# Performance work log

Hardware: AMD Instinct MI355X
Metric: run time of the kernel (lower is better)

## Reference

```python
import jax, jax.numpy as jnp
import numpy as np

B, F, T = 64, 256, 1024  # batch, input features, time steps
H, O = 1024, 512         # hidden units, output projection dim


def setup_inputs() -> dict:
    key = jax.random.key(0)
    k = jax.random.split(key, 4)
    scale_x = 1.0 / np.sqrt(F)
    scale_h = 1.0 / np.sqrt(H)
    return {
        "x": jax.random.normal(k[0], (B, F, T), dtype=jnp.float32),
        "Wx": jax.random.normal(k[1], (F, H), dtype=jnp.float32) * scale_x,
        "Wh": jax.random.normal(k[2], (H, H), dtype=jnp.float32) * scale_h,
        "b": jnp.zeros((H,), dtype=jnp.float32),
        "Wout": jax.random.normal(k[3], (H, O), dtype=jnp.float32) * scale_h,
        "bout": jnp.zeros((O,), dtype=jnp.float32),
    }


def reference(x, Wx, Wh, b, Wout, bout):
    # inputs are (B, F, T); tf.unstack(axis=-1) -> per-step (B, F) slices
    xT = jnp.moveaxis(x, -1, 0)  # (T, B, F)
    s0 = jnp.zeros((x.shape[0], Wh.shape[0]), dtype=x.dtype)

    def step(state, xt):
        # simple RNN cell: tanh(x@Wx + s@Wh + b)
        new_state = jnp.tanh(xt @ Wx + state @ Wh + b)
        return new_state, new_state

    _, states = jax.lax.scan(step, s0, xT)       # (T, B, H)
    states = jnp.moveaxis(states, 0, 1)          # (B, T, H) -- tf.stack(axis=1)
    out = states @ Wout + bout                   # per-timestep Dense projection
    return out
```

## Files before the change

### kernel.cpp

```cpp
#include <hip/hip_runtime.h>
#include <math.h>

#define B_ 64
#define F_ 256
#define T_ 1024
#define H_ 1024
#define O_ 512

#define NCHAIN 4
#define NMEM   16

#define S3_T 65536

typedef short short8 __attribute__((ext_vector_type(8)));
typedef float f32x4 __attribute__((ext_vector_type(4)));
typedef unsigned int uint4v __attribute__((ext_vector_type(4)));
typedef unsigned long long ull;

__device__ inline float bf2f(unsigned short u) {
    union { unsigned int i; float f; } v; v.i = ((unsigned int)u) << 16; return v.f;
}
__device__ inline unsigned short f2bf(float f) {
    union { float f; unsigned int i; } v; v.f = f;
    unsigned int i = v.i;
    unsigned int r = (i + 0x7fffu + ((i >> 16) & 1u)) >> 16;
    return (unsigned short)r;
}

__global__ void wt_transpose(const float* __restrict__ src,
                             unsigned short* __restrict__ dst, int K, int N) {
    __shared__ float tile[32][33];
    int n0 = blockIdx.x * 32, k0 = blockIdx.y * 32;
    int tx = threadIdx.x, ty = threadIdx.y;
    for (int i = ty; i < 32; i += 8)
        tile[i][tx] = src[(size_t)(k0 + i) * N + n0 + tx];
    __syncthreads();
    for (int i = ty; i < 32; i += 8)
        dst[(size_t)(n0 + i) * K + k0 + tx] = f2bf(tile[tx][i]);
}

__global__ void xpose_x(const float* __restrict__ x, unsigned short* __restrict__ xT) {
    __shared__ float tile[64][65];
    int id = blockIdx.x;
    int b = id >> 6;
    int ft = (id >> 4) & 3;
    int tt = id & 15;
    int f0 = ft * 64, t0 = tt * 64;
    for (int i = threadIdx.x; i < 64 * 64; i += 256) {
        int fl = i >> 6, tl = i & 63;
        tile[fl][tl] = x[((size_t)(b * F_ + f0 + fl)) * T_ + t0 + tl];
    }
    __syncthreads();
    for (int i = threadIdx.x; i < 64 * 64; i += 256) {
        int tl = i >> 6, fl = i & 63;
        xT[((size_t)(t0 + tl) * B_ + b) * F_ + f0 + fl] = f2bf(tile[fl][tl]);
    }
}

__global__ __launch_bounds__(256) void proj_kernel(
    const unsigned short* __restrict__ xT, const unsigned short* __restrict__ WxT,
    const float* __restrict__ bias, unsigned short* __restrict__ S) {
    int nb = blockIdx.x;
    int mb = blockIdx.y;
    int wave = threadIdx.x >> 6, lane = threadIdx.x & 63;
    int col16 = lane & 15, quad = lane >> 4;
    int m0 = mb * 64 + wave * 16;
    int n0 = nb * 64;

    f32x4 acc[4];
    for (int s = 0; s < 4; ++s)
        for (int r = 0; r < 4; ++r) acc[s][r] = 0.0f;

    #pragma unroll
    for (int kc = 0; kc < F_ / 32; ++kc) {
        int k0 = kc * 32 + quad * 8;
        short8 a = *reinterpret_cast<const short8*>(xT + (size_t)(m0 + col16) * F_ + k0);
        #pragma unroll
        for (int s = 0; s < 4; ++s) {
            short8 bfr = *reinterpret_cast<const short8*>(
                WxT + (size_t)(n0 + s * 16 + col16) * F_ + k0);
            acc[s] = __builtin_amdgcn_mfma_f32_16x16x32_bf16(a, bfr, acc[s], 0, 0, 0);
        }
    }
    #pragma unroll
    for (int s = 0; s < 4; ++s) {
        int col = n0 + s * 16 + col16;
        float bb = bias[col];
        #pragma unroll
        for (int r = 0; r < 4; ++r) {
            int brow = wave * 16 + quad * 4 + r;
            size_t off = (size_t)mb * S3_T + (size_t)(brow >> 4) * 16384 +
                         (size_t)(col >> 6) * 1024 + (brow & 15) * 64 + (col & 63);
            S[off] = f2bf(acc[s][r] + bb);
        }
    }
}

__global__ void init_ctrl(unsigned int* ctrl) {
    for (int i = threadIdx.x; i < 8192; i += 256) ctrl[i] = 0u;
}

template<bool LOCAL>
__device__ __forceinline__ void st_h(unsigned short* p, unsigned short v) {
    if (LOCAL) {
        *p = v;
    } else {
        asm volatile("global_store_short %0, %1, off sc0 sc1"
                     :: "v"((ull)(uintptr_t)p), "v"((unsigned int)v) : "memory");
    }
}

template<bool LOCAL>
__device__ __forceinline__ void flag_store(unsigned int* p, unsigned int v) {
    if (LOCAL) {
        asm volatile("global_atomic_swap %0, %1, off"
                     :: "v"((ull)(uintptr_t)p), "v"(v) : "memory");
    } else {
        __hip_atomic_store(p, v, __ATOMIC_RELAXED, __HIP_MEMORY_SCOPE_AGENT);
    }
}

template<bool LOCAL>
__device__ __forceinline__ unsigned int flag_load(unsigned int* p) {
    unsigned int old;
    if (LOCAL) {
        asm volatile("global_atomic_add %0, %1, %2, off sc0\n\t"
                     "s_waitcnt vmcnt(0)"
                     : "=v"(old) : "v"((ull)(uintptr_t)p), "v"(0u) : "memory");
    } else {
        old = __hip_atomic_load(p, __ATOMIC_RELAXED, __HIP_MEMORY_SCOPE_AGENT);
    }
    return old;
}

template<bool LOCAL>
__device__ void rnn_loop(unsigned short* S, const unsigned short* Bs,
                         unsigned int* ctrl, int chain, int m, int tid) {
    const int wave = tid >> 6, lane = tid & 63;
    const int col16 = lane & 15, quad = lane >> 4;
    unsigned int* myflag = &ctrl[(chain * 16 + m) * 32];

    {
        unsigned short* St0 = S + (size_t)chain * 16384 + (size_t)m * 1024;
        #pragma unroll
        for (int i = 0; i < 4; ++i) {
            int e = tid * 4 + i;
            st_h<LOCAL>(&St0[e], f2bf(tanhf(bf2f(St0[e]))));
        }
    }
    asm volatile("s_waitcnt vmcnt(0)" ::: "memory");
    __syncthreads();
    if (tid == 0) flag_store<LOCAL>(myflag, 1u);

    int dead = 0;

    for (int t = 1; t < T_; ++t) {
        unsigned short* Stb = S + (size_t)t * S3_T + (size_t)chain * 16384 + (size_t)m * 1024;
        const unsigned short* Ab = S + (size_t)(t - 1) * S3_T + (size_t)chain * 16384;

        float xp[4];
        #pragma unroll
        for (int r = 0; r < 4; ++r)
            xp[r] = bf2f(Stb[(quad * 4 + r) * 64 + wave * 16 + col16]);
        asm volatile("s_waitcnt vmcnt(0)" ::: "memory");

        if (wave == 0 && !dead) {
            const unsigned int tgt = (unsigned int)t;
            int g = 0;
            while (true) {
                unsigned int v = flag_load<LOCAL>(&ctrl[(chain * 16 + (lane & 15)) * 32]);
                if (__ballot(v >= tgt) == ~0ull) break;
                if (!LOCAL) __builtin_amdgcn_s_sleep(1);
                if (++g > (1 << 17)) { dead = 1; break; }
            }
        }
        __syncthreads();

        f32x4 acc0 = {0.f, 0.f, 0.f, 0.f};
        f32x4 acc1 = {0.f, 0.f, 0.f, 0.f};
        const unsigned short* Arow  = Ab + col16 * 64 + quad * 8;
        const unsigned short* Bslab = Bs + wave * 16384 + quad * 128 + col16 * 8;
        if (LOCAL) {
            #pragma unroll
            for (int kc2 = 0; kc2 < 16; ++kc2) {
                short8 a0 = *reinterpret_cast<const short8*>(Arow + kc2 * 1024);
                short8 a1 = *reinterpret_cast<const short8*>(Arow + kc2 * 1024 + 32);
                short8 b0 = *reinterpret_cast<const short8*>(Bslab + (2 * kc2) * 512);
                short8 b1 = *reinterpret_cast<const short8*>(Bslab + (2 * kc2 + 1) * 512);
                acc0 = __builtin_amdgcn_mfma_f32_16x16x32_bf16(a0, b0, acc0, 0, 0, 0);
                acc1 = __builtin_amdgcn_mfma_f32_16x16x32_bf16(a1, b1, acc1, 0, 0, 0);
            }
        } else {
            for (int kc2 = 0; kc2 < 16; ++kc2) {
                short8 a0, a1;
                ull p0 = (ull)(uintptr_t)(Arow + kc2 * 1024);
                ull p1 = p0 + 64;
                asm volatile("global_load_dwordx4 %0, %2, off sc0 sc1\n\t"
                             "global_load_dwordx4 %1, %3, off sc0 sc1\n\t"
                             "s_waitcnt vmcnt(0)"
                             : "=v"(a0), "=v"(a1) : "v"(p0), "v"(p1) : "memory");
                __builtin_amdgcn_sched_barrier(0);
                short8 b0 = *reinterpret_cast<const short8*>(Bslab + (2 * kc2) * 512);
                short8 b1 = *reinterpret_cast<const short8*>(Bslab + (2 * kc2 + 1) * 512);
                acc0 = __builtin_amdgcn_mfma_f32_16x16x32_bf16(a0, b0, acc0, 0, 0, 0);
                acc1 = __builtin_amdgcn_mfma_f32_16x16x32_bf16(a1, b1, acc1, 0, 0, 0);
            }
        }

        #pragma unroll
        for (int r = 0; r < 4; ++r) {
            float h = tanhf(xp[r] + acc0[r] + acc1[r]);
            st_h<LOCAL>(Stb + (quad * 4 + r) * 64 + wave * 16 + col16, f2bf(h));
        }
        asm volatile("s_waitcnt vmcnt(0)" ::: "memory");
        __syncthreads();
        if (tid == 0) flag_store<LOCAL>(myflag, (unsigned int)(t + 1));
    }
}

__global__ __launch_bounds__(256, 1) void rnn_persistent(
    unsigned short* __restrict__ S, const unsigned short* __restrict__ WhT,
    unsigned int* ctrl) {
    const int bid = blockIdx.x;
    if ((bid & 7) >= NCHAIN) return;
    const int chain = bid & 7;
    const int m = bid >> 3;
    const int tid = threadIdx.x;
    const int wave = tid >> 6, lane = tid & 63;
    const int w = chain * 16 + m;

    __shared__ unsigned short Bs[64 * 1024];
    __shared__ int s_proto;

    {
        const int n0 = m * 64;
        for (int i = tid; i < 8192; i += 256) {
            int c = i >> 7, j = i & 127;
            int kc = j >> 2, q = j & 3;
            int dst = (c >> 4) * 16384 + kc * 512 + q * 128 + (c & 15) * 8;
            *reinterpret_cast<uint4v*>(&Bs[dst]) =
                *reinterpret_cast<const uint4v*>(WhT + (size_t)(n0 + c) * 1024 + j * 8);
        }
    }

    unsigned int* flags = ctrl;
    unsigned int* ready = &ctrl[2048];
    unsigned int* xcds  = &ctrl[2560];
    unsigned int* toks  = &ctrl[5120];

    unsigned int xcd = 0;
    asm volatile("s_getreg_b32 %0, hwreg(HW_REG_XCC_ID)" : "=s"(xcd));
    if (tid == 0) {
        toks[w * 32] = (unsigned int)(w + 1);
        asm volatile("s_waitcnt vmcnt(0)" ::: "memory");
        __hip_atomic_store(&xcds[w * 32], xcd + 1u, __ATOMIC_RELAXED,
                           __HIP_MEMORY_SCOPE_AGENT);
        __hip_atomic_fetch_add(ready, 1u, __ATOMIC_RELEASE, __HIP_MEMORY_SCOPE_AGENT);
    }
    __syncthreads();

    if (tid == 0) {
        int g = 0, got = 0;
        while (true) {
            unsigned int v = __hip_atomic_load(ready, __ATOMIC_RELAXED,
                                               __HIP_MEMORY_SCOPE_AGENT);
            if (v >= 64u) { got = 1; break; }
            __builtin_amdgcn_s_sleep(2);
            if (++g > (1 << 20)) break;
        }
        s_proto = got ? -1 : 0;
    }
    __syncthreads();

    if (wave == 0) {
        int mm = lane & 15;
        unsigned int xv = __hip_atomic_load(&xcds[(chain * 16 + mm) * 32],
                                            __ATOMIC_RELAXED, __HIP_MEMORY_SCOPE_AGENT);
        unsigned int tv = toks[(chain * 16 + mm) * 32];
        unsigned int x0 = __shfl(xv, 0);
        bool uni = (__ballot(xv == x0) == ~0ull) && (x0 != 0u);
        bool tok = (__ballot(tv == (unsigned int)(chain * 16 + mm + 1)) == ~0ull);
        if (lane == 0) s_proto = (s_proto != 0 && uni && tok) ? 1 : 0;
    }
    __syncthreads();
    const int local_ok = s_proto;

    if (local_ok) rnn_loop<true>(S, Bs, ctrl, chain, m, tid);
    else          rnn_loop<false>(S, Bs, ctrl, chain, m, tid);
}

__global__ __launch_bounds__(256) void out_kernel(
    const unsigned short* __restrict__ S, const unsigned short* __restrict__ WoutT,
    const float* __restrict__ bout, float* __restrict__ out) {
    int nb = blockIdx.x;
    int tt = blockIdx.y;
    int wave = threadIdx.x >> 6, lane = threadIdx.x & 63;
    int col16 = lane & 15, quad = lane >> 4;
    int n0 = nb * 64;

    f32x4 acc[4];
    for (int s = 0; s < 4; ++s)
        for (int r = 0; r < 4; ++r) acc[s][r] = 0.0f;

    const unsigned short* arow =
        S + (size_t)tt * S3_T + (size_t)wave * 16384 + (size_t)col16 * 64 + quad * 8;

    #pragma unroll 4
    for (int kc = 0; kc < H_ / 32; ++kc) {
        int k0 = kc * 32 + quad * 8;
        short8 a = *reinterpret_cast<const short8*>(arow + (kc >> 1) * 1024 + (kc & 1) * 32);
        #pragma unroll
        for (int s = 0; s < 4; ++s) {
            short8 bfr = *reinterpret_cast<const short8*>(
                WoutT + (size_t)(n0 + s * 16 + col16) * H_ + k0);
            acc[s] = __builtin_amdgcn_mfma_f32_16x16x32_bf16(a, bfr, acc[s], 0, 0, 0);
        }
    }
    #pragma unroll
    for (int s = 0; s < 4; ++s) {
        int col = n0 + s * 16 + col16;
        float bo = bout[col];
        #pragma unroll
        for (int r = 0; r < 4; ++r) {
            int bidx = wave * 16 + quad * 4 + r;
            out[((size_t)bidx * T_ + tt) * O_ + col] = acc[s][r] + bo;
        }
    }
}

extern "C" void kernel_launch(void* const* d_in, const int* in_sizes, int n_in,
                              void* d_out, int out_size, void* d_ws, size_t ws_size,
                              hipStream_t stream) {
    const float* x    = (const float*)d_in[0];
    const float* Wx   = (const float*)d_in[1];
    const float* Wh   = (const float*)d_in[2];
    const float* bias = (const float*)d_in[3];
    const float* Wout = (const float*)d_in[4];
    const float* bout = (const float*)d_in[5];
    float* out = (float*)d_out;

    unsigned short* WhT   = (unsigned short*)d_ws;
    unsigned short* WxT   = WhT + (size_t)H_ * H_;
    unsigned short* WoutT = WxT + (size_t)H_ * F_;
    unsigned short* S     = WoutT + (size_t)O_ * H_;
    unsigned short* xT    = (unsigned short*)d_out;
    unsigned int* ctrl    = (unsigned int*)((char*)d_out + (32u << 20));

    wt_transpose<<<dim3(H_ / 32, H_ / 32), dim3(32, 8), 0, stream>>>(Wh, WhT, H_, H_);
    wt_transpose<<<dim3(H_ / 32, F_ / 32), dim3(32, 8), 0, stream>>>(Wx, WxT, F_, H_);
    wt_transpose<<<dim3(O_ / 32, H_ / 32), dim3(32, 8), 0, stream>>>(Wout, WoutT, H_, O_);
    xpose_x<<<dim3(4096), dim3(256), 0, stream>>>(x, xT);
    init_ctrl<<<1, 256, 0, stream>>>(ctrl);

    proj_kernel<<<dim3(16, 1024), dim3(256), 0, stream>>>(xT, WxT, bias, S);

    rnn_persistent<<<dim3(128), dim3(256), 0, stream>>>(S, WhT, ctrl);

    out_kernel<<<dim3(8, 1024), dim3(256), 0, stream>>>(S, WoutT, bout, out);
}
```

Baseline: 6.626 ms.

## Fan out per-consumer step flags and batch recurrent-state loads before MFMAs

Each of the 64 persistent blocks used to publish one step flag that all 16 peers in its chain polled. It now writes 16 separate flags, one per consumer, each on its own padded slot, so every consumer polls a private row. The aim is to cut contention on the shared polled lines during the per-step barrier, at the cost of 16 stores per step instead of one. The previous-step state is also loaded into 32 registers up front with a single wait, rather than a load/wait/MFMA sequence per chunk. This exposes memory-level parallelism but raises register pressure.

```diff
diff --git a/kernel.cpp b/kernel.cpp
--- a/kernel.cpp
+++ b/kernel.cpp
@@ -97,7 +97,7 @@
 }
 
 __global__ void init_ctrl(unsigned int* ctrl) {
-    for (int i = threadIdx.x; i < 8192; i += 256) ctrl[i] = 0u;
+    for (int i = threadIdx.x; i < 24576; i += 256) ctrl[i] = 0u;
 }
 
 template<bool LOCAL>
@@ -138,7 +138,7 @@
                          unsigned int* ctrl, int chain, int m, int tid) {
     const int wave = tid >> 6, lane = tid & 63;
     const int col16 = lane & 15, quad = lane >> 4;
-    unsigned int* myflag = &ctrl[(chain * 16 + m) * 32];
+    unsigned int* fan = ctrl;
 
     {
         unsigned short* St0 = S + (size_t)chain * 16384 + (size_t)m * 1024;
@@ -150,7 +150,8 @@
     }
     asm volatile("s_waitcnt vmcnt(0)" ::: "memory");
     __syncthreads();
-    if (tid == 0) flag_store<LOCAL>(myflag, 1u);
+    if (wave == 0 && lane < 16)
+        flag_store<LOCAL>(&fan[(((unsigned)chain * 16 + lane) * 16 + m) * 16], 1u);
 
     int dead = 0;
 
@@ -165,10 +166,12 @@
         asm volatile("s_waitcnt vmcnt(0)" ::: "memory");
 
         if (wave == 0 && !dead) {
-            const unsigned int tgt = (unsigned int)t;
+            const unsigned tgt = (unsigned)t;
+            unsigned int* myrow = &fan[(((unsigned)chain * 16 + m) * 16) * 16];
             int g = 0;
             while (true) {
-                unsigned int v = flag_load<LOCAL>(&ctrl[(chain * 16 + (lane & 15)) * 32]);
+                unsigned v = 0xffffffffu;
+                if (lane < 16) v = flag_load<LOCAL>(myrow + lane * 16);
                 if (__ballot(v >= tgt) == ~0ull) break;
                 if (!LOCAL) __builtin_amdgcn_s_sleep(1);
                 if (++g > (1 << 17)) { dead = 1; break; }
@@ -176,35 +179,36 @@
         }
         __syncthreads();
 
-        f32x4 acc0 = {0.f, 0.f, 0.f, 0.f};
-        f32x4 acc1 = {0.f, 0.f, 0.f, 0.f};
-        const unsigned short* Arow  = Ab + col16 * 64 + quad * 8;
-        const unsigned short* Bslab = Bs + wave * 16384 + quad * 128 + col16 * 8;
+        const unsigned short* Arow = Ab + col16 * 64 + quad * 8;
+        short8 a[32];
         if (LOCAL) {
             #pragma unroll
             for (int kc2 = 0; kc2 < 16; ++kc2) {
-                short8 a0 = *reinterpret_cast<const short8*>(Arow + kc2 * 1024);
-                short8 a1 = *reinterpret_cast<const short8*>(Arow + kc2 * 1024 + 32);
-                short8 b0 = *reinterpret_cast<const short8*>(Bslab + (2 * kc2) * 512);
-                short8 b1 = *reinterpret_cast<const short8*>(Bslab + (2 * kc2 + 1) * 512);
-                acc0 = __builtin_amdgcn_mfma_f32_16x16x32_bf16(a0, b0, acc0, 0, 0, 0);
-                acc1 = __builtin_amdgcn_mfma_f32_16x16x32_bf16(a1, b1, acc1, 0, 0, 0);
+                a[2 * kc2]     = *reinterpret_cast<const short8*>(Arow + kc2 * 1024);
+                a[2 * kc2 + 1] = *reinterpret_cast<const short8*>(Arow + kc2 * 1024 + 32);
             }
         } else {
+            #pragma unroll
             for (int kc2 = 0; kc2 < 16; ++kc2) {
-                short8 a0, a1;
                 ull p0 = (ull)(uintptr_t)(Arow + kc2 * 1024);
-                ull p1 = p0 + 64;
                 asm volatile("global_load_dwordx4 %0, %2, off sc0 sc1\n\t"
-                             "global_load_dwordx4 %1, %3, off sc0 sc1\n\t"
-                             "s_waitcnt vmcnt(0)"
-                             : "=v"(a0), "=v"(a1) : "v"(p0), "v"(p1) : "memory");
-                __builtin_amdgcn_sched_barrier(0);
-                short8 b0 = *reinterpret_cast<const short8*>(Bslab + (2 * kc2) * 512);
-                short8 b1 = *reinterpret_cast<const short8*>(Bslab + (2 * kc2 + 1) * 512);
-                acc0 = __builtin_amdgcn_mfma_f32_16x16x32_bf16(a0, b0, acc0, 0, 0, 0);
-                acc1 = __builtin_amdgcn_mfma_f32_16x16x32_bf16(a1, b1, acc1, 0, 0, 0);
+                             "global_load_dwordx4 %1, %3, off sc0 sc1"
+                             : "=v"(a[2 * kc2]), "=v"(a[2 * kc2 + 1])
+                             : "v"(p0), "v"(p0 + 64));
             }
+            asm volatile("s_waitcnt vmcnt(0)" ::: "memory");
+            __builtin_amdgcn_sched_barrier(0);
+        }
+
+        f32x4 acc0 = {0.f, 0.f, 0.f, 0.f};
+        f32x4 acc1 = {0.f, 0.f, 0.f, 0.f};
+        const unsigned short* Bslab = Bs + wave * 16384 + quad * 128 + col16 * 8;
+        #pragma unroll
+        for (int kc2 = 0; kc2 < 16; ++kc2) {
+            short8 b0 = *reinterpret_cast<const short8*>(Bslab + (2 * kc2) * 512);
+            short8 b1 = *reinterpret_cast<const short8*>(Bslab + (2 * kc2 + 1) * 512);
+            acc0 = __builtin_amdgcn_mfma_f32_16x16x32_bf16(a[2 * kc2], b0, acc0, 0, 0, 0);
+            acc1 = __builtin_amdgcn_mfma_f32_16x16x32_bf16(a[2 * kc2 + 1], b1, acc1, 0, 0, 0);
         }
 
         #pragma unroll
@@ -214,7 +218,9 @@
         }
         asm volatile("s_waitcnt vmcnt(0)" ::: "memory");
         __syncthreads();
-        if (tid == 0) flag_store<LOCAL>(myflag, (unsigned int)(t + 1));
+        if (wave == 0 && lane < 16)
+            flag_store<LOCAL>(&fan[(((unsigned)chain * 16 + lane) * 16 + m) * 16],
+                              (unsigned)(t + 1));
     }
 }
 
@@ -233,20 +239,18 @@
     __shared__ int s_proto;
 
     {
-        const int n0 = m * 64;
+        const int n0g = m * 64;
         for (int i = tid; i < 8192; i += 256) {
             int c = i >> 7, j = i & 127;
-            int kc = j >> 2, q = j & 3;
-            int dst = (c >> 4) * 16384 + kc * 512 + q * 128 + (c & 15) * 8;
+            int dst = (c >> 4) * 16384 + (j >> 2) * 512 + (j & 3) * 128 + (c & 15) * 8;
             *reinterpret_cast<uint4v*>(&Bs[dst]) =
-                *reinterpret_cast<const uint4v*>(WhT + (size_t)(n0 + c) * 1024 + j * 8);
-        }
-    }
-
-    unsigned int* flags = ctrl;
-    unsigned int* ready = &ctrl[2048];
-    unsigned int* xcds  = &ctrl[2560];
-    unsigned int* toks  = &ctrl[5120];
+                *reinterpret_cast<const uint4v*>(WhT + (size_t)(n0g + c) * 1024 + j * 8);
+        }
+    }
+
+    unsigned int* ready = &ctrl[16384];
+    unsigned int* xcds  = &ctrl[16448];
+    unsigned int* toks  = &ctrl[18496];
 
     unsigned int xcd = 0;
     asm volatile("s_getreg_b32 %0, hwreg(HW_REG_XCC_ID)" : "=s"(xcd));
```

Result: faster. 6.026 ms (-9.1%).
